# Kernel optimization log

Measured on AMD Instinct MI355X. Metric: run time of the kernel, lower is better.

Reference implementation:

```python
import jax, jax.numpy as jnp
import numpy as np

N_NODES = 50000


def setup_inputs() -> dict:
    key = jax.random.key(0)
    ks = jax.random.split(key, 6)
    F_IN, F_HID, N_EDGES = 128, 512, 800000
    x = jax.random.normal(ks[0], (N_NODES, F_IN), dtype=jnp.float32)
    edge_index = jax.random.randint(ks[1], (2, N_EDGES), 0, N_NODES, dtype=jnp.int64)
    W1 = jax.random.normal(ks[2], (F_IN, F_HID), dtype=jnp.float32) * (1.0 / np.sqrt(F_IN))
    b1 = jnp.zeros((F_HID,), dtype=jnp.float32)
    W2 = jax.random.normal(ks[3], (F_HID, F_IN), dtype=jnp.float32) * (1.0 / np.sqrt(F_HID))
    b2 = jnp.zeros((F_IN,), dtype=jnp.float32)
    eps = jnp.zeros((), dtype=jnp.float32)  # train_eps=True, init 0
    return {"x": x, "edge_index": edge_index, "W1": W1, "b1": b1, "W2": W2, "b2": b2, "eps": eps}


def reference(x, edge_index, W1, b1, W2, b2, eps):
    # GINConv: out = MLP((1+eps)*x + sum_{j in N(i)} x_j)
    src, dst = edge_index[0], edge_index[1]
    agg = jax.ops.segment_sum(x[src], dst, num_segments=N_NODES)  # [N, F]
    h = (1.0 + eps) * x + agg
    h = jax.nn.relu(h @ W1 + b1)
    out = h @ W2 + b2
    return out
```

## Files before the change

kernel.cpp:

```cpp
#include <hip/hip_runtime.h>
#include <hip/hip_bf16.h>

#define N_NODES 50000
#define F_IN    128
#define F_HID   512
#define N_EDGES 800000

#define NBKT 782
#define NREP 8
#define RCAP 256
#define NDMAX 64

typedef __bf16 bf16x2 __attribute__((ext_vector_type(2)));
typedef __bf16 bf16x4 __attribute__((ext_vector_type(4)));
typedef __bf16 bf16x8 __attribute__((ext_vector_type(8)));
typedef float  f32x4  __attribute__((ext_vector_type(4)));
typedef unsigned short u16x8 __attribute__((ext_vector_type(8)));

#define NB_E 782
#define NB_X 6250
#define NB_W 32
__global__ __launch_bounds__(256) void prep_fill(const float* __restrict__ x,
                                                 const int* __restrict__ ei,
                                                 const float* __restrict__ W1,
                                                 const float* __restrict__ W2,
                                                 __bf16* __restrict__ xb,
                                                 __bf16* __restrict__ w1f,
                                                 __bf16* __restrict__ w2f,
                                                 int* __restrict__ bcnt,
                                                 int* __restrict__ entries) {
    int b = blockIdx.x, tid = threadIdx.x;
    if (b < NB_E) {
        int e0 = (b * 256 + tid) * 4;
        int rep = b & (NREP - 1);
        if (e0 + 4 <= N_EDGES) {
            int4 s4 = *(const int4*)&ei[e0];
            int4 d4 = *(const int4*)&ei[N_EDGES + e0];
            int c0 = (d4.x >> 6) * NREP + rep;
            int c1 = (d4.y >> 6) * NREP + rep;
            int c2 = (d4.z >> 6) * NREP + rep;
            int c3 = (d4.w >> 6) * NREP + rep;
            int p0 = atomicAdd(&bcnt[c0 * 16], 1);
            int p1 = atomicAdd(&bcnt[c1 * 16], 1);
            int p2 = atomicAdd(&bcnt[c2 * 16], 1);
            int p3 = atomicAdd(&bcnt[c3 * 16], 1);
            if (p0 < RCAP) entries[(size_t)c0 * RCAP + p0] = ((d4.x & 63) << 16) | s4.x;
            if (p1 < RCAP) entries[(size_t)c1 * RCAP + p1] = ((d4.y & 63) << 16) | s4.y;
            if (p2 < RCAP) entries[(size_t)c2 * RCAP + p2] = ((d4.z & 63) << 16) | s4.z;
            if (p3 < RCAP) entries[(size_t)c3 * RCAP + p3] = ((d4.w & 63) << 16) | s4.w;
        } else {
            for (int k = 0; k < 4; ++k) {
                int e = e0 + k;
                if (e < N_EDGES) {
                    int src = ei[e], dst = ei[N_EDGES + e];
                    int c = (dst >> 6) * NREP + rep;
                    int p = atomicAdd(&bcnt[c * 16], 1);
                    if (p < RCAP) entries[(size_t)c * RCAP + p] = ((dst & 63) << 16) | src;
                }
            }
        }
    } else if (b < NB_E + NB_X) {
        int i = (b - NB_E) * 256 + tid;
        float4 v = ((const float4*)x)[i];
        bf16x4 o = {(__bf16)v.x, (__bf16)v.y, (__bf16)v.z, (__bf16)v.w};
        ((bf16x4*)xb)[i] = o;
    } else if (b < NB_E + NB_X + NB_W) {
        int t = (b - NB_E - NB_X) * 256 + tid;
        int lane = t & 63, kk = (t >> 6) & 3, nt = (t >> 8) & 7, c = (t >> 11) & 3;
        int q = lane >> 4, l16 = lane & 15;
        bf16x8 o;
        #pragma unroll
        for (int j = 0; j < 8; ++j)
            o[j] = (__bf16)W1[(kk * 32 + q * 8 + j) * F_HID + c * 128 + nt * 16 + l16];
        *(bf16x8*)(w1f + (size_t)t * 8) = o;
    } else {
        int t = (b - NB_E - NB_X - NB_W) * 256 + tid;
        int lane = t & 63, kk = (t >> 6) & 3, nt = (t >> 8) & 7, c = (t >> 11) & 3;
        int q = lane >> 4, l16 = lane & 15;
        bf16x8 o;
        #pragma unroll
        for (int j = 0; j < 8; ++j)
            o[j] = (__bf16)W2[(c * 128 + kk * 32 + q * 8 + j) * F_IN + nt * 16 + l16];
        *(bf16x8*)(w2f + (size_t)t * 8) = o;
    }
}

__global__ __launch_bounds__(512) void gin_fused(const __bf16* __restrict__ xb,
                                                 const int* __restrict__ bcnt,
                                                 const int* __restrict__ entries,
                                                 const float* __restrict__ eps,
                                                 const __bf16* __restrict__ w1f,
                                                 const __bf16* __restrict__ w2f,
                                                 const float* __restrict__ b1,
                                                 const float* __restrict__ b2,
                                                 float* __restrict__ out) {
    __shared__ union __attribute__((aligned(16))) {
        struct { int degs[64]; unsigned short bin16[64 * NDMAX]; } p0;
        __bf16 Hb[8192];
    } u;
    __shared__ __attribute__((aligned(16))) __bf16 As[8192];

    const int tid = threadIdx.x;
    const int wave = tid >> 6, lane = tid & 63;
    const int q = lane >> 4, l16 = lane & 15;
    const int bkt = blockIdx.x;

    if (tid < 64) u.p0.degs[tid] = 0;
    __syncthreads();

    {
        int cell = bkt * NREP + wave;
        int cnt = bcnt[cell * 16];
        cnt = cnt < RCAP ? cnt : RCAP;
        const int* eb = entries + (size_t)cell * RCAP;
        for (int i = lane; i < cnt; i += 64) {
            int en = eb[i];
            int dl = en >> 16;
            int p = atomicAdd(&u.p0.degs[dl], 1);
            if (p < NDMAX)
                u.p0.bin16[dl * NDMAX + (p & 3) * 16 + (p >> 2)] =
                    (unsigned short)(en & 0xffff);
        }
    }
    __syncthreads();

    const float s = 1.0f + eps[0];
    const __bf16 z0 = (__bf16)0.0f;
    const bf16x8 Z8 = {z0, z0, z0, z0, z0, z0, z0, z0};
#define ROW(idx) (*(const bf16x8*)(xb + (size_t)(idx) * F_IN + l16 * 8))
#define IDX(u_) ((u_) < 8 ? I0[(u_) & 7] : I1[(u_) & 7])
    #pragma unroll 2
    for (int t = 0; t < 8; ++t) {
        int n = wave * 8 + t;
        int node = bkt * 64 + n;
        int dg = u.p0.degs[n];
        dg = dg < NDMAX ? dg : NDMAX;
        int myc = (dg + 3 - q) >> 2;
        u16x8 I0 = *(const u16x8*)&u.p0.bin16[n * NDMAX + q * 16];
        u16x8 I1 = *(const u16x8*)&u.p0.bin16[n * NDMAX + q * 16 + 8];

        float acc[8];
        #pragma unroll
        for (int i = 0; i < 8; ++i) acc[i] = 0.0f;
        if (q == 0) {
            bf16x8 self = ROW(node);
            #pragma unroll
            for (int i = 0; i < 8; ++i) acc[i] = (float)self[i] * s;
        }

        #pragma unroll
        for (int u0 = 0; u0 < 16; u0 += 4) {
            if (myc > u0) {
                bf16x8 r0 = Z8, r1 = Z8, r2 = Z8, r3 = Z8;
                r0 = ROW(IDX(u0));
                if (myc > u0 + 1) r1 = ROW(IDX(u0 + 1));
                if (myc > u0 + 2) r2 = ROW(IDX(u0 + 2));
                if (myc > u0 + 3) r3 = ROW(IDX(u0 + 3));
                #pragma unroll
                for (int i = 0; i < 8; ++i)
                    acc[i] += ((float)r0[i] + (float)r1[i]) + ((float)r2[i] + (float)r3[i]);
            }
        }

        #pragma unroll
        for (int i = 0; i < 8; ++i) {
            acc[i] += __shfl_xor(acc[i], 16);
            acc[i] += __shfl_xor(acc[i], 32);
        }
        if (lane < 16) {
            int g = n >> 4, r16 = n & 15;
            bf16x8 o;
            #pragma unroll
            for (int i = 0; i < 8; ++i) o[i] = (__bf16)acc[i];
            int byte = (g * 16 + lane) * 256 + r16 * 16;
            byte ^= (lane & 7) << 4;
            *(bf16x8*)((char*)As + byte) = o;
        }
    }
    __syncthreads();

    const int wr = wave >> 2, wc = wave & 3;

    f32x4 acc_o[2][2];
    #pragma unroll
    for (int ni = 0; ni < 2; ++ni) {
        float bv = b2[wc * 32 + ni * 16 + l16];
        f32x4 b4 = {bv, bv, bv, bv};
        acc_o[0][ni] = b4;
        acc_o[1][ni] = b4;
    }

    for (int c = 0; c < 4; ++c) {
        f32x4 acc_h[2][2];
        #pragma unroll
        for (int ni = 0; ni < 2; ++ni) {
            float bv = b1[c * 128 + wc * 32 + ni * 16 + l16];
            f32x4 b4 = {bv, bv, bv, bv};
            acc_h[0][ni] = b4;
            acc_h[1][ni] = b4;
        }
        #pragma unroll
        for (int kk = 0; kk < 4; ++kk) {
            bf16x8 am[2], bw[2];
            #pragma unroll
            for (int mi = 0; mi < 2; ++mi) {
                int g = wr * 2 + mi;
                int byte = ((g * 4 + kk) * 4 + q) * 256 + l16 * 16;
                byte ^= ((kk * 4 + q) & 7) << 4;
                am[mi] = *(const bf16x8*)((const char*)As + byte);
            }
            #pragma unroll
            for (int ni = 0; ni < 2; ++ni)
                bw[ni] = *(const bf16x8*)(w1f +
                    ((size_t)((c * 8 + wc * 2 + ni) * 4 + kk) << 9) + lane * 8);
            #pragma unroll
            for (int mi = 0; mi < 2; ++mi)
                #pragma unroll
                for (int ni = 0; ni < 2; ++ni)
                    acc_h[mi][ni] = __builtin_amdgcn_mfma_f32_16x16x32_bf16(
                        am[mi], bw[ni], acc_h[mi][ni], 0, 0, 0);
        }
        #pragma unroll
        for (int mi = 0; mi < 2; ++mi) {
            int g = wr * 2 + mi;
            #pragma unroll
            for (int ni = 0; ni < 2; ++ni)
                #pragma unroll
                for (int r = 0; r < 4; ++r)
                    u.Hb[(((g * 4 + wc) * 64 + (ni * 2 + (l16 >> 3)) * 16 + q * 4 + r) << 3)
                         + (l16 & 7)] = (__bf16)fmaxf(acc_h[mi][ni][r], 0.0f);
        }
        __syncthreads();

        #pragma unroll
        for (int kk = 0; kk < 4; ++kk) {
            bf16x8 am[2], bw[2];
            #pragma unroll
            for (int mi = 0; mi < 2; ++mi)
                am[mi] = *(const bf16x8*)&u.Hb[(((wr * 2 + mi) * 4 + kk) * 64 + lane) << 3];
            #pragma unroll
            for (int ni = 0; ni < 2; ++ni)
                bw[ni] = *(const bf16x8*)(w2f +
                    ((size_t)((c * 8 + wc * 2 + ni) * 4 + kk) << 9) + lane * 8);
            #pragma unroll
            for (int mi = 0; mi < 2; ++mi)
                #pragma unroll
                for (int ni = 0; ni < 2; ++ni)
                    acc_o[mi][ni] = __builtin_amdgcn_mfma_f32_16x16x32_bf16(
                        am[mi], bw[ni], acc_o[mi][ni], 0, 0, 0);
        }
        __syncthreads();
    }

    const int m0 = bkt * 64;
    #pragma unroll
    for (int mi = 0; mi < 2; ++mi)
        #pragma unroll
        for (int ni = 0; ni < 2; ++ni)
            #pragma unroll
            for (int r = 0; r < 4; ++r) {
                int m = m0 + wr * 32 + mi * 16 + q * 4 + r;
                if (m < N_NODES)
                    out[(size_t)m * F_IN + wc * 32 + ni * 16 + l16] = acc_o[mi][ni][r];
            }
}

extern "C" void kernel_launch(void* const* d_in, const int* in_sizes, int n_in,
                              void* d_out, int out_size, void* d_ws, size_t ws_size,
                              hipStream_t stream) {
    const float* x   = (const float*)d_in[0];
    const int*   ei  = (const int*)d_in[1];
    const float* W1  = (const float*)d_in[2];
    const float* b1  = (const float*)d_in[3];
    const float* W2  = (const float*)d_in[4];
    const float* b2  = (const float*)d_in[5];
    const float* eps = (const float*)d_in[6];
    float* out = (float*)d_out;

    char* ws = (char*)d_ws;
    __bf16* xb   = (__bf16*)ws;
    __bf16* w1f  = (__bf16*)(ws + 12800000);
    __bf16* w2f  = (__bf16*)(ws + 13000000);
    int*    bcnt = (int*)(ws + 13200000);
    int*    entries = (int*)(ws + 13700000);

    hipMemsetAsync(bcnt, 0, NBKT * NREP * 64, stream);
    prep_fill<<<NB_E + NB_X + 2 * NB_W, 256, 0, stream>>>(x, ei, W1, W2,
                                                          xb, w1f, w2f, bcnt, entries);
    gin_fused<<<NBKT, 512, 0, stream>>>(xb, bcnt, entries, eps, w1f, w2f, b1, b2, out);
}
```

Before: 182.1 us.

## Use zero-padding sentinel row for branchless neighbor gathers; split fill and prep kernels

Neighbor-index bins in shared memory are pre-filled with a sentinel index pointing to a zeroed padding row placed after xb. The first eight gathers per lane then run unconditionally, giving the compiler independent loads with no branches. Only the tail beyond eight uses guarded loads. The edge-bucketing pass is split from the x/W conversion into its own kernel, and an extra memset zeroes the padding rows. This adds wasted loads for low-degree nodes, one more launch and one more memset.

```diff
diff --git a/kernel.cpp b/kernel.cpp
--- a/kernel.cpp
+++ b/kernel.cpp
@@ -10,6 +10,7 @@
 #define NREP 8
 #define RCAP 256
 #define NDMAX 64
+#define NZERO 50000
 
 typedef __bf16 bf16x2 __attribute__((ext_vector_type(2)));
 typedef __bf16 bf16x4 __attribute__((ext_vector_type(4)));
@@ -18,54 +19,56 @@
 typedef unsigned short u16x8 __attribute__((ext_vector_type(8)));
 
 #define NB_E 782
+__global__ __launch_bounds__(256) void fillk(const int* __restrict__ ei,
+                                             int* __restrict__ bcnt,
+                                             int* __restrict__ entries) {
+    int b = blockIdx.x, tid = threadIdx.x;
+    int e0 = (b * 256 + tid) * 4;
+    int rep = b & (NREP - 1);
+    if (e0 + 4 <= N_EDGES) {
+        int4 s4 = *(const int4*)&ei[e0];
+        int4 d4 = *(const int4*)&ei[N_EDGES + e0];
+        int c0 = (d4.x >> 6) * NREP + rep;
+        int c1 = (d4.y >> 6) * NREP + rep;
+        int c2 = (d4.z >> 6) * NREP + rep;
+        int c3 = (d4.w >> 6) * NREP + rep;
+        int p0 = atomicAdd(&bcnt[c0 * 16], 1);
+        int p1 = atomicAdd(&bcnt[c1 * 16], 1);
+        int p2 = atomicAdd(&bcnt[c2 * 16], 1);
+        int p3 = atomicAdd(&bcnt[c3 * 16], 1);
+        if (p0 < RCAP) entries[(size_t)c0 * RCAP + p0] = ((d4.x & 63) << 16) | s4.x;
+        if (p1 < RCAP) entries[(size_t)c1 * RCAP + p1] = ((d4.y & 63) << 16) | s4.y;
+        if (p2 < RCAP) entries[(size_t)c2 * RCAP + p2] = ((d4.z & 63) << 16) | s4.z;
+        if (p3 < RCAP) entries[(size_t)c3 * RCAP + p3] = ((d4.w & 63) << 16) | s4.w;
+    } else {
+        for (int k = 0; k < 4; ++k) {
+            int e = e0 + k;
+            if (e < N_EDGES) {
+                int src = ei[e], dst = ei[N_EDGES + e];
+                int c = (dst >> 6) * NREP + rep;
+                int p = atomicAdd(&bcnt[c * 16], 1);
+                if (p < RCAP) entries[(size_t)c * RCAP + p] = ((dst & 63) << 16) | src;
+            }
+        }
+    }
+}
+
 #define NB_X 6250
 #define NB_W 32
-__global__ __launch_bounds__(256) void prep_fill(const float* __restrict__ x,
-                                                 const int* __restrict__ ei,
-                                                 const float* __restrict__ W1,
-                                                 const float* __restrict__ W2,
-                                                 __bf16* __restrict__ xb,
-                                                 __bf16* __restrict__ w1f,
-                                                 __bf16* __restrict__ w2f,
-                                                 int* __restrict__ bcnt,
-                                                 int* __restrict__ entries) {
+__global__ __launch_bounds__(256) void prep(const float* __restrict__ x,
+                                            const float* __restrict__ W1,
+                                            const float* __restrict__ W2,
+                                            __bf16* __restrict__ xb,
+                                            __bf16* __restrict__ w1f,
+                                            __bf16* __restrict__ w2f) {
     int b = blockIdx.x, tid = threadIdx.x;
-    if (b < NB_E) {
-        int e0 = (b * 256 + tid) * 4;
-        int rep = b & (NREP - 1);
-        if (e0 + 4 <= N_EDGES) {
-            int4 s4 = *(const int4*)&ei[e0];
-            int4 d4 = *(const int4*)&ei[N_EDGES + e0];
-            int c0 = (d4.x >> 6) * NREP + rep;
-            int c1 = (d4.y >> 6) * NREP + rep;
-            int c2 = (d4.z >> 6) * NREP + rep;
-            int c3 = (d4.w >> 6) * NREP + rep;
-            int p0 = atomicAdd(&bcnt[c0 * 16], 1);
-            int p1 = atomicAdd(&bcnt[c1 * 16], 1);
-            int p2 = atomicAdd(&bcnt[c2 * 16], 1);
-            int p3 = atomicAdd(&bcnt[c3 * 16], 1);
-            if (p0 < RCAP) entries[(size_t)c0 * RCAP + p0] = ((d4.x & 63) << 16) | s4.x;
-            if (p1 < RCAP) entries[(size_t)c1 * RCAP + p1] = ((d4.y & 63) << 16) | s4.y;
-            if (p2 < RCAP) entries[(size_t)c2 * RCAP + p2] = ((d4.z & 63) << 16) | s4.z;
-            if (p3 < RCAP) entries[(size_t)c3 * RCAP + p3] = ((d4.w & 63) << 16) | s4.w;
-        } else {
-            for (int k = 0; k < 4; ++k) {
-                int e = e0 + k;
-                if (e < N_EDGES) {
-                    int src = ei[e], dst = ei[N_EDGES + e];
-                    int c = (dst >> 6) * NREP + rep;
-                    int p = atomicAdd(&bcnt[c * 16], 1);
-                    if (p < RCAP) entries[(size_t)c * RCAP + p] = ((dst & 63) << 16) | src;
-                }
-            }
-        }
-    } else if (b < NB_E + NB_X) {
-        int i = (b - NB_E) * 256 + tid;
+    if (b < NB_X) {
+        int i = b * 256 + tid;
         float4 v = ((const float4*)x)[i];
         bf16x4 o = {(__bf16)v.x, (__bf16)v.y, (__bf16)v.z, (__bf16)v.w};
         ((bf16x4*)xb)[i] = o;
-    } else if (b < NB_E + NB_X + NB_W) {
-        int t = (b - NB_E - NB_X) * 256 + tid;
+    } else if (b < NB_X + NB_W) {
+        int t = (b - NB_X) * 256 + tid;
         int lane = t & 63, kk = (t >> 6) & 3, nt = (t >> 8) & 7, c = (t >> 11) & 3;
         int q = lane >> 4, l16 = lane & 15;
         bf16x8 o;
@@ -74,7 +77,7 @@
             o[j] = (__bf16)W1[(kk * 32 + q * 8 + j) * F_HID + c * 128 + nt * 16 + l16];
         *(bf16x8*)(w1f + (size_t)t * 8) = o;
     } else {
-        int t = (b - NB_E - NB_X - NB_W) * 256 + tid;
+        int t = (b - NB_X - NB_W) * 256 + tid;
         int lane = t & 63, kk = (t >> 6) & 3, nt = (t >> 8) & 7, c = (t >> 11) & 3;
         int q = lane >> 4, l16 = lane & 15;
         bf16x8 o;
@@ -106,6 +109,12 @@
     const int bkt = blockIdx.x;
 
     if (tid < 64) u.p0.degs[tid] = 0;
+    {
+        const int zz = (NZERO << 16) | NZERO;
+        int* b32 = (int*)u.p0.bin16;
+        #pragma unroll
+        for (int k = 0; k < 4; ++k) b32[tid * 4 + k] = zz;
+    }
     __syncthreads();
 
     {
@@ -125,10 +134,7 @@
     __syncthreads();
 
     const float s = 1.0f + eps[0];
-    const __bf16 z0 = (__bf16)0.0f;
-    const bf16x8 Z8 = {z0, z0, z0, z0, z0, z0, z0, z0};
 #define ROW(idx) (*(const bf16x8*)(xb + (size_t)(idx) * F_IN + l16 * 8))
-#define IDX(u_) ((u_) < 8 ? I0[(u_) & 7] : I1[(u_) & 7])
     #pragma unroll 2
     for (int t = 0; t < 8; ++t) {
         int n = wave * 8 + t;
@@ -148,18 +154,23 @@
             for (int i = 0; i < 8; ++i) acc[i] = (float)self[i] * s;
         }
 
-        #pragma unroll
-        for (int u0 = 0; u0 < 16; u0 += 4) {
-            if (myc > u0) {
-                bf16x8 r0 = Z8, r1 = Z8, r2 = Z8, r3 = Z8;
-                r0 = ROW(IDX(u0));
-                if (myc > u0 + 1) r1 = ROW(IDX(u0 + 1));
-                if (myc > u0 + 2) r2 = ROW(IDX(u0 + 2));
-                if (myc > u0 + 3) r3 = ROW(IDX(u0 + 3));
-                #pragma unroll
-                for (int i = 0; i < 8; ++i)
-                    acc[i] += ((float)r0[i] + (float)r1[i]) + ((float)r2[i] + (float)r3[i]);
-            }
+        bf16x8 ra0 = ROW(I0[0]), ra1 = ROW(I0[1]), ra2 = ROW(I0[2]), ra3 = ROW(I0[3]);
+        bf16x8 rb0 = ROW(I0[4]), rb1 = ROW(I0[5]), rb2 = ROW(I0[6]), rb3 = ROW(I0[7]);
+        #pragma unroll
+        for (int i = 0; i < 8; ++i)
+            acc[i] += ((float)ra0[i] + (float)ra1[i]) + ((float)ra2[i] + (float)ra3[i]);
+        #pragma unroll
+        for (int i = 0; i < 8; ++i)
+            acc[i] += ((float)rb0[i] + (float)rb1[i]) + ((float)rb2[i] + (float)rb3[i]);
+
+        if (myc > 8) {
+            #pragma unroll
+            for (int v = 0; v < 8; ++v)
+                if (myc > 8 + v) {
+                    bf16x8 r = ROW(I1[v]);
+                    #pragma unroll
+                    for (int i = 0; i < 8; ++i) acc[i] += (float)r[i];
+                }
         }
 
         #pragma unroll
@@ -279,13 +290,14 @@
 
     char* ws = (char*)d_ws;
     __bf16* xb   = (__bf16*)ws;
-    __bf16* w1f  = (__bf16*)(ws + 12800000);
-    __bf16* w2f  = (__bf16*)(ws + 13000000);
-    int*    bcnt = (int*)(ws + 13200000);
-    int*    entries = (int*)(ws + 13700000);
+    __bf16* w1f  = (__bf16*)(ws + 12900000);
+    __bf16* w2f  = (__bf16*)(ws + 13100000);
+    int*    bcnt = (int*)(ws + 13300000);
+    int*    entries = (int*)(ws + 13800000);
 
     hipMemsetAsync(bcnt, 0, NBKT * NREP * 64, stream);
-    prep_fill<<<NB_E + NB_X + 2 * NB_W, 256, 0, stream>>>(x, ei, W1, W2,
-                                                          xb, w1f, w2f, bcnt, entries);
+    hipMemsetAsync((char*)ws + (size_t)N_NODES * F_IN * 2, 0, 48 * F_IN * 2, stream);
+    fillk<<<NB_E, 256, 0, stream>>>(ei, bcnt, entries);
+    prep<<<NB_X + 2 * NB_W, 256, 0, stream>>>(x, W1, W2, xb, w1f, w2f);
     gin_fused<<<NBKT, 512, 0, stream>>>(xb, bcnt, entries, eps, w1f, w2f, b1, b2, out);
 }
```

Result: slower. 187.4 us (+2.9%).
